# Performance work log

Measured on AMD Instinct MI355X. Metric: run time of the kernel, lower is better.

Reference implementation:

```python
import jax, jax.numpy as jnp
import numpy as np

B, T, D = 8, 2048, 1024
EPS = 1e-5

def _layernorm(x, g, b):
    mu = jnp.mean(x, axis=-1, keepdims=True)
    var = jnp.mean(jnp.square(x - mu), axis=-1, keepdims=True)
    return (x - mu) * jax.lax.rsqrt(var + EPS) * g + b

def setup_inputs() -> dict:
    key = jax.random.key(0)
    ks = jax.random.split(key, 8)
    scale = 1.0 / np.sqrt(D)
    text_inputs = jax.random.normal(ks[0], (B, T, D), dtype=jnp.float32)
    sit_mask = jax.random.randint(ks[1], (B, T), 0, 2).astype(jnp.float32)
    Wq = jax.random.normal(ks[2], (D, D), dtype=jnp.float32) * scale
    Wk = jax.random.normal(ks[3], (D, D), dtype=jnp.float32) * scale
    Wv = jax.random.normal(ks[4], (D, D), dtype=jnp.float32) * scale
    Wf1 = jax.random.normal(ks[5], (D, D), dtype=jnp.float32) * scale
    bf1 = jnp.zeros((D,), dtype=jnp.float32)
    Wf2 = jax.random.normal(ks[6], (D, D), dtype=jnp.float32) * scale
    bf2 = jnp.zeros((D,), dtype=jnp.float32)
    ln1_g = jnp.ones((D,), dtype=jnp.float32)
    ln1_b = jnp.zeros((D,), dtype=jnp.float32)
    ln2_g = jnp.ones((D,), dtype=jnp.float32)
    ln2_b = jnp.zeros((D,), dtype=jnp.float32)
    return dict(text_inputs=text_inputs, sit_mask=sit_mask, Wq=Wq, Wk=Wk, Wv=Wv,
                ln1_g=ln1_g, ln1_b=ln1_b, Wf1=Wf1, bf1=bf1, Wf2=Wf2, bf2=bf2,
                ln2_g=ln2_g, ln2_b=ln2_b)

def reference(text_inputs, sit_mask, Wq, Wk, Wv, ln1_g, ln1_b, Wf1, bf1, Wf2, bf2, ln2_g, ln2_b):
    x = text_inputs  # [B,T,D]
    d = x.shape[-1]
    # torch Linear: y = x @ W.T
    q = jnp.einsum('btd,ed->bte', x, Wq)
    k = jnp.einsum('btd,ed->bte', x, Wk)
    v = jnp.einsum('btd,ed->bte', x, Wv)
    # scaled scores with causal (strictly-upper = -inf) mask
    scores = jnp.einsum('btd,bsd->bts', q, k) / jnp.sqrt(jnp.asarray(d, x.dtype))
    causal = jnp.tril(jnp.ones((x.shape[1], x.shape[1]), dtype=bool))  # keep diag + past
    scores = jnp.where(causal[None], scores, -jnp.inf)
    attn = jax.nn.softmax(scores, axis=-1)
    # per-batch SIT padding mask applied AFTER softmax (rows may not sum to 1)
    pad_keep = (sit_mask[:, :, None] * sit_mask[:, None, :]) != 0  # [B,T,T]
    attn = jnp.where(pad_keep, attn, 0.0)
    att_out = jnp.einsum('bts,bsd->btd', attn, v)
    # residual + LN, FFN (Linear-ReLU-Linear), residual + LN
    h = _layernorm(att_out + x, ln1_g, ln1_b)
    ff = jnp.einsum('btd,ed->bte', jax.nn.relu(jnp.einsum('btd,ed->bte', h, Wf1) + bf1), Wf2) + bf2
    out = _layernorm(ff + h, ln2_g, ln2_b)
    return out
```

## Files before the change

### kernel.cpp

```cpp
#include <hip/hip_runtime.h>

typedef unsigned short ushort_t;
typedef __attribute__((ext_vector_type(8))) __bf16 bf16x8;
typedef __attribute__((ext_vector_type(4))) float f32x4;
typedef __attribute__((ext_vector_type(4))) int i32x4;
typedef __attribute__((ext_vector_type(4))) unsigned short u16x4;
typedef __attribute__((ext_vector_type(8))) unsigned short u16x8;

__device__ __forceinline__ float bf2f(ushort_t u) {
  union { unsigned u32; float f; } c; c.u32 = ((unsigned)u) << 16; return c.f;
}
__device__ __forceinline__ ushort_t f2bf(float f) {
  union { float f; unsigned u32; } c; c.f = f;
  unsigned u = c.u32;
  u += 0x7fffu + ((u >> 16) & 1u);
  return (ushort_t)(u >> 16);
}

__device__ __forceinline__ void gload_lds16(const void* g, void* l) {
  __builtin_amdgcn_global_load_lds(
      (const __attribute__((address_space(1))) void*)g,
      (__attribute__((address_space(3))) void*)l,
      16, 0, 0);
}

__device__ __forceinline__ void stage_half(const char* gbase, long row0, int ldbytes,
                                           int kbyte, char* lds_half, int tid)
{
  const int rl = tid >> 3;
  const int cs = ((tid & 7) ^ (rl & 7)) << 4;
  const char* g0 = gbase + (row0 + rl) * (long)ldbytes + kbyte + cs;
  char* l0 = lds_half + ((tid >> 6) << 10);
  gload_lds16(g0, l0);
  gload_lds16(g0 + (long)ldbytes * 64, l0 + 8192);
}

#define BAR() __builtin_amdgcn_s_barrier()
#define VMW4() asm volatile("s_waitcnt vmcnt(4)" ::: "memory")
#define VMW6() asm volatile("s_waitcnt vmcnt(6)" ::: "memory")
#define PR1() __builtin_amdgcn_s_setprio(1)
#define PR0() __builtin_amdgcn_s_setprio(0)

#define READ_A(dst, Abase, mb) \
  _Pragma("unroll") for (int m_ = 0; m_ < 4; ++m_) { \
    const char* p_ = (Abase) + ((wr << 7) + (mb) + m_ * 16 + fr) * 128; \
    dst[m_][0] = *(const bf16x8*)(p_ + ch0); \
    dst[m_][1] = *(const bf16x8*)(p_ + ch1); }

#define READ_B4(dst, Bbase, jb) \
  _Pragma("unroll") for (int n_ = 0; n_ < 2; ++n_) { \
    const char* p_ = (Bbase) + ((wc << 6) + (jb) + n_ * 16 + fr) * 128; \
    dst[n_][0] = *(const bf16x8*)(p_ + ch0); \
    dst[n_][1] = *(const bf16x8*)(p_ + ch1); }

#define MFMA_Q(ib, jb, aarr, barr) \
  _Pragma("unroll") for (int m_ = 0; m_ < 4; ++m_) \
  _Pragma("unroll") for (int n_ = 0; n_ < 2; ++n_) \
  _Pragma("unroll") for (int s_ = 0; s_ < 2; ++s_) \
    acc[(ib) + m_][(jb) + n_] = __builtin_amdgcn_mfma_f32_16x16x32_bf16( \
        aarr[m_][s_], barr[n_][s_], acc[(ib) + m_][(jb) + n_], 0, 0, 0);

#define STAGE_A(t, h, db) stage_half(gA, m0 + (h) * 128, ldab, (t) << 7, \
    (char*)lds + (db) * 32768 + (h) * 16384, tid)
#define STAGE_B(t, h, db) stage_half(gB, n0 + (h) * 128, ldbb, (t) << 7, \
    (char*)lds + 65536 + (db) * 32768 + (h) * 16384, tid)

template<int EPI, int MAPQ, bool ROUTE>
__global__ __launch_bounds__(512, 1) void gemm256(
    const ushort_t* __restrict__ A, int lda,
    const ushort_t* __restrict__ B, int ldb,
    ushort_t* __restrict__ C0, ushort_t* __restrict__ C1, ushort_t* __restrict__ C2,
    int ldc, const float* __restrict__ bias, float scale, int K)
{
  __shared__ __attribute__((aligned(16))) ushort_t lds[65536];

  int bx, by;
  if (MAPQ == 1) {
    const int flat = blockIdx.y * 4 + blockIdx.x;
    by = ((flat >> 5) << 3) | (flat & 7);
    bx = (flat >> 3) & 3;
  } else if (MAPQ == 2) {
    const int l = blockIdx.x;
    const int c = l & 7, u = l >> 3;
    const int q12 = u / 12;
    by = (q12 << 3) | c;
    bx = u - q12 * 12;
  } else { bx = blockIdx.x; by = blockIdx.y; }

  const int NT = K >> 6;
  const int NIT = NT >> 1, NTm1 = NT - 1;

  const int tid = threadIdx.x;
  const int lane = tid & 63, fr = lane & 15, g = lane >> 4, lm = lane & 7;
  const int wv = tid >> 6, wr = wv >> 2, wc = wv & 3;
  const long m0 = (long)by << 8, n0 = (long)bx << 8;

  const char* gA = (const char*)A;
  const char* gB = (const char*)B;
  const int ldab = lda << 1, ldbb = ldb << 1;

  const int ch0 = (g ^ lm) << 4;
  const int ch1 = ((4 | g) ^ lm) << 4;

  const char* A0 = (const char*)lds;
  const char* A1 = (const char*)lds + 32768;
  const char* B0 = (const char*)lds + 65536;
  const char* B1 = (const char*)lds + 98304;

  f32x4 acc[8][4] = {};
  bf16x8 aF[4][2], aG[4][2], bX[2][2];

  STAGE_A(0, 0, 0); STAGE_A(0, 1, 0); STAGE_B(0, 0, 0); STAGE_B(0, 1, 0);
  STAGE_A(1, 0, 1); STAGE_A(1, 1, 1);
  VMW4(); BAR();

  for (int i = 0; i < NIT; ++i) {
    const int t1 = 2 * i + 1;
    const int t2 = (2 * i + 2 < NTm1) ? 2 * i + 2 : NTm1;
    const int t3 = (2 * i + 3 < NTm1) ? 2 * i + 3 : NTm1;

    READ_A(aF, A0, 0); READ_B4(bX, B0, 0);
    STAGE_B(t1, 0, 1);
    BAR(); PR1(); MFMA_Q(0, 0, aF, bX); PR0(); BAR();

    READ_A(aG, A0, 64);
    STAGE_B(t1, 1, 1);
    BAR(); PR1(); MFMA_Q(4, 0, aG, bX); PR0(); BAR();

    READ_B4(bX, B0, 32);
    STAGE_A(t2, 0, 0);
    BAR(); PR1(); MFMA_Q(4, 2, aG, bX); PR0(); BAR();

    STAGE_A(t2, 1, 0);
    BAR(); PR1(); MFMA_Q(0, 2, aF, bX); PR0(); VMW4(); BAR();

    READ_A(aF, A1, 0); READ_B4(bX, B1, 0);
    STAGE_B(t2, 0, 0);
    BAR(); PR1(); MFMA_Q(0, 0, aF, bX); PR0(); BAR();

    READ_A(aG, A1, 64);
    STAGE_B(t2, 1, 0);
    BAR(); PR1(); MFMA_Q(4, 0, aG, bX); PR0(); BAR();

    READ_B4(bX, B1, 32);
    STAGE_A(t3, 0, 1);
    BAR(); PR1(); MFMA_Q(4, 2, aG, bX); PR0(); BAR();

    STAGE_A(t3, 1, 1);
    BAR(); PR1(); MFMA_Q(0, 2, aF, bX); PR0(); VMW4(); BAR();
  }

  ushort_t* Cd = C0;
  long nc0 = (long)bx << 8;
  if constexpr (ROUTE) {
    const int which = bx >> 2;
    Cd = (which == 0) ? C0 : (which == 1) ? C1 : C2;
    nc0 = (long)(bx & 3) << 8;
  }

  const int cm = g << 2, cn = fr;
#pragma unroll
  for (int i2 = 0; i2 < 8; ++i2)
#pragma unroll
    for (int j2 = 0; j2 < 4; ++j2) {
      const long gm = m0 + (wr << 7) + i2 * 16 + cm;
      const long gn = nc0 + (wc << 6) + j2 * 16 + cn;
      float bv = 0.f;
      if constexpr (EPI >= 1) bv = bias[gn];
#pragma unroll
      for (int r = 0; r < 4; ++r) {
        float v = acc[i2][j2][r] * scale + bv;
        if constexpr (EPI == 2) v = fmaxf(v, 0.f);
        Cd[(gm + r) * ldc + gn] = f2bf(v);
      }
    }
}

#define RDA4(dst, base, ch) \
  _Pragma("unroll") for (int m_ = 0; m_ < 4; ++m_) \
    dst[m_] = *(const bf16x8*)((base) + ((wr4 << 6) + m_ * 16 + fr) * 128 + (ch));

#define RDB4(dst, base, ch) \
  _Pragma("unroll") for (int n_ = 0; n_ < 4; ++n_) \
    dst[n_] = *(const bf16x8*)((base) + ((wc2 << 6) + n_ * 16 + fr) * 128 + (ch));

#define MM16() \
  _Pragma("unroll") for (int m_ = 0; m_ < 4; ++m_) \
  _Pragma("unroll") for (int n_ = 0; n_ < 4; ++n_) \
    acc[m_][n_] = __builtin_amdgcn_mfma_f32_16x16x32_bf16( \
        af[m_], bfv[n_], acc[m_][n_], 0, 0, 0);

#define SA2_(t, dst) do { \
    stage_half(gA, m0, ldab, (t) << 7, (dst), tid); \
    stage_half(gA, m0 + 128, ldab, (t) << 7, (dst) + 16384, tid); } while (0)
#define SB2_(t, dst) stage_half(gB, n0, ldbb, (t) << 7, (dst), tid)

template<int EPI, int MAP, bool CKLIM>
__global__ __launch_bounds__(512, 1) void gemmA(
    const ushort_t* __restrict__ A, int lda, long bsA,
    const ushort_t* __restrict__ B, int ldb, long bsB,
    ushort_t* __restrict__ C, int ldc, long bsC,
    const float* __restrict__ bias, float scale, int K)
{
  __shared__ __attribute__((aligned(16))) ushort_t lds[73728];

  int bx, by, bz;
  if (MAP == 1) {
    const int bid = blockIdx.x;
    bz = bid & 7; const int r = bid >> 3;
    by = 0; while ((by + 1) * (by + 2) <= r) ++by;
    bx = r - by * (by + 1);
  } else if (MAP == 2) {
    const int bid = blockIdx.x;
    bz = bid & 7; const int u = bid >> 3;
    by = 7 - (u >> 3); bx = u & 7;
  } else { bx = blockIdx.x; by = blockIdx.y; bz = blockIdx.z; }

  const int NT = CKLIM ? ((by + 1) << 2) : (K >> 6);

  const int tid = threadIdx.x;
  const int lane = tid & 63, fr = lane & 15, g = lane >> 4, lm = lane & 7;
  const int wv = tid >> 6;
  const int wr4 = wv >> 1, wc2 = wv & 1;
  const long m0 = (long)by << 8, n0 = (long)bx << 7;

  const char* gA = (const char*)(A + bz * bsA);
  const char* gB = (const char*)(B + bz * bsB);
  const int ldab = lda << 1, ldbb = ldb << 1;

  const int ch0 = (g ^ lm) << 4;
  const int ch1 = ((4 | g) ^ lm) << 4;

  char* a0 = (char*)lds;
  char* b0 = a0 + 32768;
  char* a1 = a0 + 49152;
  char* b1 = a1 + 32768;
  char* a2 = a0 + 98304;
  char* b2 = a2 + 32768;

  f32x4 acc[4][4] = {};
  bf16x8 af[4], bfv[4];

  SA2_(0, a0); SB2_(0, b0);
  SA2_(1, a1); SB2_(1, b1);
  VMW6(); BAR();

  for (int u = 0; u < NT; ++u) {
    const int t2 = (u + 2 < NT) ? u + 2 : NT - 1;
    RDA4(af, a0, ch0); RDB4(bfv, b0, ch0);
    SA2_(t2, a2); SB2_(t2, b2);
    BAR(); PR1(); MM16(); PR0(); BAR();
    RDA4(af, a0, ch1); RDB4(bfv, b0, ch1);
    VMW6(); BAR(); PR1(); MM16(); PR0(); BAR();
    char* ta = a0; a0 = a1; a1 = a2; a2 = ta;
    char* tb = b0; b0 = b1; b1 = b2; b2 = tb;
  }

  ushort_t* Cb = C + bz * bsC;
  const int cm = g << 2, cn = fr;
#pragma unroll
  for (int i2 = 0; i2 < 4; ++i2)
#pragma unroll
    for (int j2 = 0; j2 < 4; ++j2) {
      const long gm = m0 + (wr4 << 6) + i2 * 16 + cm;
      const long gn = n0 + (wc2 << 6) + j2 * 16 + cn;
      float bv = 0.f;
      if constexpr (EPI >= 1) bv = bias[gn];
#pragma unroll
      for (int r = 0; r < 4; ++r) {
        float v = acc[i2][j2][r] * scale + bv;
        if constexpr (EPI == 2) v = fmaxf(v, 0.f);
        Cb[(gm + r) * ldc + gn] = f2bf(v);
      }
    }
}

__global__ __launch_bounds__(256) void transpose_bf16(
    const ushort_t* __restrict__ V, int ldv, long bsV,
    ushort_t* __restrict__ Vt, int ldt, long bsT)
{
  __shared__ __attribute__((aligned(16))) ushort_t tile[64][72];
  const int bz = blockIdx.z;
  const ushort_t* Vb = V + bz * bsV;
  ushort_t* Tb = Vt + bz * bsT;
  const long s0 = (long)blockIdx.y << 6;
  const long d0 = (long)blockIdx.x << 6;
  const int tid = threadIdx.x;
  const int r = tid >> 3, c = tid & 7;
#pragma unroll
  for (int h = 0; h < 2; ++h) {
    const int rr = r + h * 32;
    i32x4 v = *(const i32x4*)(Vb + (s0 + rr) * ldv + d0 + c * 8);
    *(i32x4*)&tile[rr][c * 8] = v;
  }
  __syncthreads();
#pragma unroll
  for (int h = 0; h < 2; ++h) {
    const int dr = r + h * 32;
    union { ushort_t u[8]; i32x4 v; } t;
#pragma unroll
    for (int j = 0; j < 8; ++j) t.u[j] = tile[c * 8 + j][dr];
    *(i32x4*)(Tb + (d0 + dr) * ldt + s0 + c * 8) = t.v;
  }
}

__global__ __launch_bounds__(256) void softmax_sit(ushort_t* __restrict__ S,
                                                   const float* __restrict__ sit)
{
  __shared__ float red[4];
  const long row = blockIdx.x;
  const int b = (int)(row >> 11);
  const int t = (int)(row & 2047);
  const int n = t + 1;
  const int rup = ((t >> 8) + 1) << 8;
  ushort_t* Srow = S + (row << 11);
  const int tid = threadIdx.x;
  const int i0 = tid << 3;
  const bool act = i0 < rup;

  u16x8 raw = {};
  if (act) raw = *(const u16x8*)(Srow + i0);
  float v[8];
#pragma unroll
  for (int j = 0; j < 8; ++j) v[j] = bf2f(raw[j]);

  float mloc = -3.0e38f;
#pragma unroll
  for (int j = 0; j < 8; ++j) if (i0 + j < n) mloc = fmaxf(mloc, v[j]);
#pragma unroll
  for (int o = 32; o > 0; o >>= 1) mloc = fmaxf(mloc, __shfl_down(mloc, o, 64));
  if ((tid & 63) == 0) red[tid >> 6] = mloc;
  __syncthreads();
  const float m = fmaxf(fmaxf(red[0], red[1]), fmaxf(red[2], red[3]));
  __syncthreads();

  float e[8];
  float sloc = 0.f;
#pragma unroll
  for (int j = 0; j < 8; ++j) {
    e[j] = (i0 + j < n) ? __expf(v[j] - m) : 0.f;
    sloc += e[j];
  }
#pragma unroll
  for (int o = 32; o > 0; o >>= 1) sloc += __shfl_down(sloc, o, 64);
  if ((tid & 63) == 0) red[tid >> 6] = sloc;
  __syncthreads();
  const float l = red[0] + red[1] + red[2] + red[3];

  float inv = 1.f / l;
  if (sit[row] == 0.f) inv = 0.f;
  if (act) {
    const float* sitb = sit + ((long)b << 11) + i0;
    u16x8 out;
#pragma unroll
    for (int j = 0; j < 8; ++j) {
      const float p = (i0 + j < n && sitb[j] != 0.f) ? e[j] * inv : 0.f;
      out[j] = f2bf(p);
    }
    *(u16x8*)(Srow + i0) = out;
  }
}

template<bool RES_F32, bool OUT_F32>
__global__ __launch_bounds__(256) void resid_ln(
    const ushort_t* __restrict__ xin, const void* __restrict__ resv,
    const float* __restrict__ g, const float* __restrict__ be, void* __restrict__ outv)
{
  __shared__ float red[4];
  const long base = (long)blockIdx.x << 10;
  const int tid = threadIdx.x;
  const int i0 = tid << 2;

  const u16x4 xa = *(const u16x4*)(xin + base + i0);
  float v[4];
  if constexpr (RES_F32) {
    const float4 rv = *(const float4*)((const float*)resv + base + i0);
    v[0] = bf2f(xa.x) + rv.x; v[1] = bf2f(xa.y) + rv.y;
    v[2] = bf2f(xa.z) + rv.z; v[3] = bf2f(xa.w) + rv.w;
  } else {
    const u16x4 rb = *(const u16x4*)((const ushort_t*)resv + base + i0);
    v[0] = bf2f(xa.x) + bf2f(rb.x); v[1] = bf2f(xa.y) + bf2f(rb.y);
    v[2] = bf2f(xa.z) + bf2f(rb.z); v[3] = bf2f(xa.w) + bf2f(rb.w);
  }
  float s = v[0] + v[1] + v[2] + v[3];
#pragma unroll
  for (int o = 32; o > 0; o >>= 1) s += __shfl_down(s, o, 64);
  if ((tid & 63) == 0) red[tid >> 6] = s;
  __syncthreads();
  const float mu = (red[0] + red[1] + red[2] + red[3]) * (1.f / 1024.f);
  __syncthreads();
  float s2 = 0.f;
#pragma unroll
  for (int j = 0; j < 4; ++j) { const float d = v[j] - mu; s2 += d * d; }
#pragma unroll
  for (int o = 32; o > 0; o >>= 1) s2 += __shfl_down(s2, o, 64);
  if ((tid & 63) == 0) red[tid >> 6] = s2;
  __syncthreads();
  const float rstd = rsqrtf((red[0] + red[1] + red[2] + red[3]) * (1.f / 1024.f) + 1e-5f);

  const float4 gv = *(const float4*)(g + i0);
  const float4 bv = *(const float4*)(be + i0);
  const float o0 = (v[0] - mu) * rstd * gv.x + bv.x;
  const float o1 = (v[1] - mu) * rstd * gv.y + bv.y;
  const float o2 = (v[2] - mu) * rstd * gv.z + bv.z;
  const float o3 = (v[3] - mu) * rstd * gv.w + bv.w;
  if constexpr (OUT_F32) {
    float4 ov; ov.x = o0; ov.y = o1; ov.z = o2; ov.w = o3;
    *(float4*)((float*)outv + base + i0) = ov;
  } else {
    u16x4 ob = { f2bf(o0), f2bf(o1), f2bf(o2), f2bf(o3) };
    *(u16x4*)((ushort_t*)outv + base + i0) = ob;
  }
}

__global__ __launch_bounds__(256) void cast_f32_bf16(const float* __restrict__ src,
                                                     ushort_t* __restrict__ dst, int n4)
{
  const int i = blockIdx.x * 256 + threadIdx.x;
  if (i >= n4) return;
  const float4 v = *(const float4*)(src + ((long)i << 2));
  u16x4 o = { f2bf(v.x), f2bf(v.y), f2bf(v.z), f2bf(v.w) };
  *(u16x4*)(dst + ((long)i << 2)) = o;
}

__global__ __launch_bounds__(256) void cast_w5(
    const float* __restrict__ s0, const float* __restrict__ s1,
    const float* __restrict__ s2, const float* __restrict__ s3,
    const float* __restrict__ s4, ushort_t* __restrict__ dst)
{
  const int w = blockIdx.y;
  const float* src = (w == 0) ? s0 : (w == 1) ? s1 : (w == 2) ? s2 : (w == 3) ? s3 : s4;
  const long off = (long)w << 20;
  const int i = blockIdx.x * 256 + threadIdx.x;
  const float4 v = *(const float4*)(src + ((long)i << 2));
  u16x4 o = { f2bf(v.x), f2bf(v.y), f2bf(v.z), f2bf(v.w) };
  *(u16x4*)(dst + off + ((long)i << 2)) = o;
}

extern "C" void kernel_launch(void* const* d_in, const int* in_sizes, int n_in,
                              void* d_out, int out_size, void* d_ws, size_t ws_size,
                              hipStream_t stream) {
  const int T = 2048, D = 1024;
  const long TD = (long)T * D;
  const long ND = 8 * TD;
  const float* x    = (const float*)d_in[0];
  const float* sit  = (const float*)d_in[1];
  const float* Wq   = (const float*)d_in[2];
  const float* Wk   = (const float*)d_in[3];
  const float* Wv   = (const float*)d_in[4];
  const float* ln1g = (const float*)d_in[5];
  const float* ln1b = (const float*)d_in[6];
  const float* Wf1  = (const float*)d_in[7];
  const float* bf1  = (const float*)d_in[8];
  const float* Wf2  = (const float*)d_in[9];
  const float* bf2  = (const float*)d_in[10];
  const float* ln2g = (const float*)d_in[11];
  const float* ln2b = (const float*)d_in[12];

  ushort_t* W16 = (ushort_t*)d_ws;
  ushort_t* xb  = W16;
  ushort_t* vb  = W16 + ND;
  ushort_t* S   = W16;
  ushort_t* hb  = W16;
  ushort_t* ff1 = W16 + ND;
  ushort_t* vt  = W16 + 2 * ND;
  ushort_t* ff2 = vt;
  ushort_t* wq  = W16 + 3 * ND;
  ushort_t* wf1 = wq + 3L * D * D;
  ushort_t* wf2 = wf1 + (long)D * D;
  ushort_t* qb = (ushort_t*)d_out;
  ushort_t* kb = qb + ND;
  ushort_t* attb = (ushort_t*)d_out;

  cast_f32_bf16<<<16384, 256, 0, stream>>>(x, xb, (int)(ND / 4));
  cast_w5<<<dim3(1024, 5), 256, 0, stream>>>(Wq, Wk, Wv, Wf1, Wf2, wq);

  gemm256<0, 2, true><<<dim3(768), 512, 0, stream>>>(
      xb, 1024, wq, 1024, qb, kb, vb, 1024, nullptr, 1.f, 1024);

  transpose_bf16<<<dim3(16, 32, 8), 256, 0, stream>>>(vb, 1024, TD, vt, 2048, TD);

  gemmA<0, 1, false><<<dim3(576), 512, 0, stream>>>(
      qb, 1024, TD, kb, 1024, TD, S, 2048, (long)T * T, nullptr, 0.03125f, 1024);

  softmax_sit<<<16384, 256, 0, stream>>>(S, sit);

  gemmA<0, 2, true><<<dim3(512), 512, 0, stream>>>(
      S, 2048, (long)T * T, vt, 2048, TD, attb, 1024, TD, nullptr, 1.f, 2048);

  resid_ln<true, false><<<16384, 256, 0, stream>>>(attb, x, ln1g, ln1b, hb);

  gemm256<2, 1, false><<<dim3(4, 64), 512, 0, stream>>>(
      hb, 1024, wf1, 1024, ff1, ff1, ff1, 1024, bf1, 1.f, 1024);
  gemm256<1, 1, false><<<dim3(4, 64), 512, 0, stream>>>(
      ff1, 1024, wf2, 1024, ff2, ff2, ff2, 1024, bf2, 1.f, 1024);

  resid_ln<false, true><<<16384, 256, 0, stream>>>(ff2, hb, ln2g, ln2b, (float*)d_out);
}
```

Before: 395.6 us.

## Switch GEMM kernels to 32x32x16 MFMA with restructured software pipeline

Both GEMM kernels (the QKV/FFN gemm256 and the batched attention gemmA) move from 16x16x32 to 32x32x16 bf16 MFMA tiles. This lowers LDS fragment reads per FLOP and raises arithmetic intensity per instruction. The main loops are reordered so LDS fragment reads for the next quarter overlap the current MFMA group, and fragments are prefetched across barriers. Epilogues are rewritten for the 32x32 accumulator layout. The cost is higher register pressure and some risk in the new pipeline's waitcnt and barrier ordering, for example vmcnt(0) in gemm256.

```diff
diff --git a/kernel.cpp b/kernel.cpp
--- a/kernel.cpp
+++ b/kernel.cpp
@@ -2,6 +2,7 @@
 
 typedef unsigned short ushort_t;
 typedef __attribute__((ext_vector_type(8))) __bf16 bf16x8;
+typedef __attribute__((ext_vector_type(16))) float f32x16;
 typedef __attribute__((ext_vector_type(4))) float f32x4;
 typedef __attribute__((ext_vector_type(4))) int i32x4;
 typedef __attribute__((ext_vector_type(4))) unsigned short u16x4;
@@ -36,34 +37,28 @@
 }
 
 #define BAR() __builtin_amdgcn_s_barrier()
+#define VMW0() asm volatile("s_waitcnt vmcnt(0)" ::: "memory")
 #define VMW4() asm volatile("s_waitcnt vmcnt(4)" ::: "memory")
 #define VMW6() asm volatile("s_waitcnt vmcnt(6)" ::: "memory")
 #define PR1() __builtin_amdgcn_s_setprio(1)
 #define PR0() __builtin_amdgcn_s_setprio(0)
 
-#define READ_A(dst, Abase, mb) \
-  _Pragma("unroll") for (int m_ = 0; m_ < 4; ++m_) { \
-    const char* p_ = (Abase) + ((wr << 7) + (mb) + m_ * 16 + fr) * 128; \
-    dst[m_][0] = *(const bf16x8*)(p_ + ch0); \
-    dst[m_][1] = *(const bf16x8*)(p_ + ch1); }
-
-#define READ_B4(dst, Bbase, jb) \
-  _Pragma("unroll") for (int n_ = 0; n_ < 2; ++n_) { \
-    const char* p_ = (Bbase) + ((wc << 6) + (jb) + n_ * 16 + fr) * 128; \
-    dst[n_][0] = *(const bf16x8*)(p_ + ch0); \
-    dst[n_][1] = *(const bf16x8*)(p_ + ch1); }
-
-#define MFMA_Q(ib, jb, aarr, barr) \
-  _Pragma("unroll") for (int m_ = 0; m_ < 4; ++m_) \
-  _Pragma("unroll") for (int n_ = 0; n_ < 2; ++n_) \
-  _Pragma("unroll") for (int s_ = 0; s_ < 2; ++s_) \
-    acc[(ib) + m_][(jb) + n_] = __builtin_amdgcn_mfma_f32_16x16x32_bf16( \
-        aarr[m_][s_], barr[n_][s_], acc[(ib) + m_][(jb) + n_], 0, 0, 0);
-
-#define STAGE_A(t, h, db) stage_half(gA, m0 + (h) * 128, ldab, (t) << 7, \
-    (char*)lds + (db) * 32768 + (h) * 16384, tid)
-#define STAGE_B(t, h, db) stage_half(gB, n0 + (h) * 128, ldbb, (t) << 7, \
-    (char*)lds + 65536 + (db) * 32768 + (h) * 16384, tid)
+#define G_RA(dst, base, rb) \
+  _Pragma("unroll") for (int f_ = 0; f_ < 2; ++f_) \
+  _Pragma("unroll") for (int s_ = 0; s_ < 4; ++s_) \
+    dst[f_][s_] = *(const bf16x8*)((base) + ((rb) + f_ * 32 + l31) * 128 + ch[s_]);
+#define G_RB(dst, base, cb) \
+  _Pragma("unroll") for (int s_ = 0; s_ < 4; ++s_) \
+    dst[s_] = *(const bf16x8*)((base) + ((cb) + l31) * 128 + ch[s_]);
+#define G_MM(r0, nf, Aa, Bb) \
+  _Pragma("unroll") for (int s_ = 0; s_ < 4; ++s_) \
+  _Pragma("unroll") for (int f_ = 0; f_ < 2; ++f_) \
+    acc[(r0) + f_][nf] = __builtin_amdgcn_mfma_f32_32x32x16_bf16( \
+        Aa[f_][s_], Bb[s_], acc[(r0) + f_][nf], 0, 0, 0);
+#define SAE_(t, hh) stage_half(gA, m0 + (hh) * 128, ldab, (t) << 7, AE + (hh) * 16384, tid)
+#define SAO_(t, hh) stage_half(gA, m0 + (hh) * 128, ldab, (t) << 7, AO + (hh) * 16384, tid)
+#define SBE_(t, hh) stage_half(gB, n0 + (hh) * 128, ldbb, (t) << 7, BE + (hh) * 16384, tid)
+#define SBO_(t, hh) stage_half(gB, n0 + (hh) * 128, ldbb, (t) << 7, BO + (hh) * 16384, tid)
 
 template<int EPI, int MAPQ, bool ROUTE>
 __global__ __launch_bounds__(512, 1) void gemm256(
@@ -87,67 +82,68 @@
     bx = u - q12 * 12;
   } else { bx = blockIdx.x; by = blockIdx.y; }
 
-  const int NT = K >> 6;
-  const int NIT = NT >> 1, NTm1 = NT - 1;
-
-  const int tid = threadIdx.x;
-  const int lane = tid & 63, fr = lane & 15, g = lane >> 4, lm = lane & 7;
+  const int NT = K >> 6, NIT = NT >> 1, NTm1 = NT - 1;
+
+  const int tid = threadIdx.x, lane = tid & 63;
+  const int l31 = lane & 31, lm = lane & 7, h = lane >> 5;
   const int wv = tid >> 6, wr = wv >> 2, wc = wv & 3;
+  const int wrb = wr << 7, wcb = wc << 6;
   const long m0 = (long)by << 8, n0 = (long)bx << 8;
 
   const char* gA = (const char*)A;
   const char* gB = (const char*)B;
   const int ldab = lda << 1, ldbb = ldb << 1;
 
-  const int ch0 = (g ^ lm) << 4;
-  const int ch1 = ((4 | g) ^ lm) << 4;
-
-  const char* A0 = (const char*)lds;
-  const char* A1 = (const char*)lds + 32768;
-  const char* B0 = (const char*)lds + 65536;
-  const char* B1 = (const char*)lds + 98304;
-
-  f32x4 acc[8][4] = {};
-  bf16x8 aF[4][2], aG[4][2], bX[2][2];
-
-  STAGE_A(0, 0, 0); STAGE_A(0, 1, 0); STAGE_B(0, 0, 0); STAGE_B(0, 1, 0);
-  STAGE_A(1, 0, 1); STAGE_A(1, 1, 1);
+  int ch[4];
+#pragma unroll
+  for (int s = 0; s < 4; ++s) ch[s] = ((((s << 1) | h) ^ lm) << 4);
+
+  char* AE = (char*)lds;
+  char* AO = AE + 32768;
+  char* BE = AE + 65536;
+  char* BO = AE + 98304;
+
+  f32x16 acc[4][2] = {};
+  bf16x8 aF[2][4], aG[2][4], bL[4], bL2[4], bH[4];
+
+  SAE_(0, 0); SAE_(0, 1); SBE_(0, 0); SBE_(0, 1);
+  SAO_(1, 0); SAO_(1, 1);
   VMW4(); BAR();
+  G_RA(aF, AE, wrb); G_RB(bL, BE, wcb);
 
   for (int i = 0; i < NIT; ++i) {
-    const int t1 = 2 * i + 1;
+    const int tO = (2 * i + 1 < NTm1) ? 2 * i + 1 : NTm1;
     const int t2 = (2 * i + 2 < NTm1) ? 2 * i + 2 : NTm1;
     const int t3 = (2 * i + 3 < NTm1) ? 2 * i + 3 : NTm1;
 
-    READ_A(aF, A0, 0); READ_B4(bX, B0, 0);
-    STAGE_B(t1, 0, 1);
-    BAR(); PR1(); MFMA_Q(0, 0, aF, bX); PR0(); BAR();
-
-    READ_A(aG, A0, 64);
-    STAGE_B(t1, 1, 1);
-    BAR(); PR1(); MFMA_Q(4, 0, aG, bX); PR0(); BAR();
-
-    READ_B4(bX, B0, 32);
-    STAGE_A(t2, 0, 0);
-    BAR(); PR1(); MFMA_Q(4, 2, aG, bX); PR0(); BAR();
-
-    STAGE_A(t2, 1, 0);
-    BAR(); PR1(); MFMA_Q(0, 2, aF, bX); PR0(); VMW4(); BAR();
-
-    READ_A(aF, A1, 0); READ_B4(bX, B1, 0);
-    STAGE_B(t2, 0, 0);
-    BAR(); PR1(); MFMA_Q(0, 0, aF, bX); PR0(); BAR();
-
-    READ_A(aG, A1, 64);
-    STAGE_B(t2, 1, 0);
-    BAR(); PR1(); MFMA_Q(4, 0, aG, bX); PR0(); BAR();
-
-    READ_B4(bX, B1, 32);
-    STAGE_A(t3, 0, 1);
-    BAR(); PR1(); MFMA_Q(4, 2, aG, bX); PR0(); BAR();
-
-    STAGE_A(t3, 1, 1);
-    BAR(); PR1(); MFMA_Q(0, 2, aF, bX); PR0(); VMW4(); BAR();
+    PR1(); G_MM(0, 0, aF, bL); PR0();
+    G_RB(bH, BE, wcb + 32);
+    SBO_(tO, 0);
+    BAR();
+    PR1(); G_MM(0, 1, aF, bH); PR0();
+    G_RA(aG, AE, wrb + 64);
+    SBO_(tO, 1);
+    BAR();
+    PR1(); G_MM(2, 1, aG, bH); PR0();
+    BAR();
+    PR1(); G_MM(2, 0, aG, bL); PR0();
+    VMW0(); BAR();
+    G_RA(aF, AO, wrb); G_RB(bL2, BO, wcb);
+    SAE_(t2, 0); SAE_(t2, 1);
+    PR1(); G_MM(0, 0, aF, bL2); PR0();
+    G_RB(bH, BO, wcb + 32);
+    SBE_(t2, 0);
+    BAR();
+    PR1(); G_MM(0, 1, aF, bH); PR0();
+    G_RA(aG, AO, wrb + 64);
+    SBE_(t2, 1);
+    BAR();
+    PR1(); G_MM(2, 1, aG, bH); PR0();
+    BAR();
+    PR1(); G_MM(2, 0, aG, bL2); PR0();
+    VMW0(); BAR();
+    G_RA(aF, AE, wrb); G_RB(bL, BE, wcb);
+    SAO_(t3, 0); SAO_(t3, 1);
   }
 
   ushort_t* Cd = C0;
@@ -158,42 +154,34 @@
     nc0 = (long)(bx & 3) << 8;
   }
 
-  const int cm = g << 2, cn = fr;
-#pragma unroll
-  for (int i2 = 0; i2 < 8; ++i2)
-#pragma unroll
-    for (int j2 = 0; j2 < 4; ++j2) {
-      const long gm = m0 + (wr << 7) + i2 * 16 + cm;
-      const long gn = nc0 + (wc << 6) + j2 * 16 + cn;
+  const int rb4 = h << 2;
+#pragma unroll
+  for (int mf = 0; mf < 4; ++mf)
+#pragma unroll
+    for (int nf = 0; nf < 2; ++nf) {
+      const long gmb = m0 + wrb + mf * 32;
+      const long gn = nc0 + wcb + nf * 32 + l31;
       float bv = 0.f;
       if constexpr (EPI >= 1) bv = bias[gn];
 #pragma unroll
-      for (int r = 0; r < 4; ++r) {
-        float v = acc[i2][j2][r] * scale + bv;
+      for (int r = 0; r < 16; ++r) {
+        const int row = (r & 3) + 8 * (r >> 2) + rb4;
+        float v = acc[mf][nf][r] * scale + bv;
         if constexpr (EPI == 2) v = fmaxf(v, 0.f);
-        Cd[(gm + r) * ldc + gn] = f2bf(v);
+        Cd[(gmb + row) * ldc + gn] = f2bf(v);
       }
     }
 }
 
-#define RDA4(dst, base, ch) \
-  _Pragma("unroll") for (int m_ = 0; m_ < 4; ++m_) \
-    dst[m_] = *(const bf16x8*)((base) + ((wr4 << 6) + m_ * 16 + fr) * 128 + (ch));
-
-#define RDB4(dst, base, ch) \
-  _Pragma("unroll") for (int n_ = 0; n_ < 4; ++n_) \
-    dst[n_] = *(const bf16x8*)((base) + ((wc2 << 6) + n_ * 16 + fr) * 128 + (ch));
-
-#define MM16() \
-  _Pragma("unroll") for (int m_ = 0; m_ < 4; ++m_) \
-  _Pragma("unroll") for (int n_ = 0; n_ < 4; ++n_) \
-    acc[m_][n_] = __builtin_amdgcn_mfma_f32_16x16x32_bf16( \
-        af[m_], bfv[n_], acc[m_][n_], 0, 0, 0);
-
-#define SA2_(t, dst) do { \
-    stage_half(gA, m0, ldab, (t) << 7, (dst), tid); \
-    stage_half(gA, m0 + 128, ldab, (t) << 7, (dst) + 16384, tid); } while (0)
-#define SB2_(t, dst) stage_half(gB, n0, ldbb, (t) << 7, (dst), tid)
+#define A_RA(dst, base, rb) \
+  _Pragma("unroll") for (int s_ = 0; s_ < 4; ++s_) \
+    dst[s_] = *(const bf16x8*)((base) + ((rb) + l31) * 128 + ch[s_]);
+#define A_MM(mh, nh, Aa, Bb) \
+  _Pragma("unroll") for (int s_ = 0; s_ < 4; ++s_) \
+    acc[mh][nh] = __builtin_amdgcn_mfma_f32_32x32x16_bf16( \
+        Aa[s_], Bb[s_], acc[mh][nh], 0, 0, 0);
+#define SAA_(t, hh, dst) stage_half(gA, m0 + (hh) * 128, ldab, (t) << 7, (dst) + (hh) * 16384, tid)
+#define SBA_(t, dst) stage_half(gB, n0, ldbb, (t) << 7, (dst), tid)
 
 template<int EPI, int MAP, bool CKLIM>
 __global__ __launch_bounds__(512, 1) void gemmA(
@@ -217,60 +205,86 @@
   } else { bx = blockIdx.x; by = blockIdx.y; bz = blockIdx.z; }
 
   const int NT = CKLIM ? ((by + 1) << 2) : (K >> 6);
-
-  const int tid = threadIdx.x;
-  const int lane = tid & 63, fr = lane & 15, g = lane >> 4, lm = lane & 7;
-  const int wv = tid >> 6;
-  const int wr4 = wv >> 1, wc2 = wv & 1;
+  const int NIT = NT >> 1, NTm1 = NT - 1;
+
+  const int tid = threadIdx.x, lane = tid & 63;
+  const int l31 = lane & 31, lm = lane & 7, h = lane >> 5;
+  const int wv = tid >> 6, wr4 = wv >> 1, wc2 = wv & 1;
+  const int wrb = wr4 << 6, wcb = wc2 << 6;
   const long m0 = (long)by << 8, n0 = (long)bx << 7;
 
   const char* gA = (const char*)(A + bz * bsA);
   const char* gB = (const char*)(B + bz * bsB);
   const int ldab = lda << 1, ldbb = ldb << 1;
 
-  const int ch0 = (g ^ lm) << 4;
-  const int ch1 = ((4 | g) ^ lm) << 4;
-
-  char* a0 = (char*)lds;
-  char* b0 = a0 + 32768;
-  char* a1 = a0 + 49152;
-  char* b1 = a1 + 32768;
-  char* a2 = a0 + 98304;
-  char* b2 = a2 + 32768;
-
-  f32x4 acc[4][4] = {};
-  bf16x8 af[4], bfv[4];
-
-  SA2_(0, a0); SB2_(0, b0);
-  SA2_(1, a1); SB2_(1, b1);
+  int ch[4];
+#pragma unroll
+  for (int s = 0; s < 4; ++s) ch[s] = ((((s << 1) | h) ^ lm) << 4);
+
+  char* pA0 = (char*)lds;          char* pB0 = pA0 + 32768;
+  char* pA1 = (char*)lds + 49152;  char* pB1 = pA1 + 32768;
+  char* pA2 = (char*)lds + 98304;  char* pB2 = pA2 + 32768;
+
+  f32x16 acc[2][2] = {};
+  bf16x8 aF[4], aG[4], bL[4], bL2[4], bH[4];
+
+  SAA_(0, 0, pA0); SAA_(0, 1, pA0); SBA_(0, pB0);
+  SAA_(1, 0, pA1); SAA_(1, 1, pA1); SBA_(1, pB1);
   VMW6(); BAR();
-
-  for (int u = 0; u < NT; ++u) {
-    const int t2 = (u + 2 < NT) ? u + 2 : NT - 1;
-    RDA4(af, a0, ch0); RDB4(bfv, b0, ch0);
-    SA2_(t2, a2); SB2_(t2, b2);
-    BAR(); PR1(); MM16(); PR0(); BAR();
-    RDA4(af, a0, ch1); RDB4(bfv, b0, ch1);
-    VMW6(); BAR(); PR1(); MM16(); PR0(); BAR();
-    char* ta = a0; a0 = a1; a1 = a2; a2 = ta;
-    char* tb = b0; b0 = b1; b1 = b2; b2 = tb;
+  A_RA(aF, pA0, wrb); A_RA(bL, pB0, wcb);
+
+  for (int i = 0; i < NIT; ++i) {
+    const int t2 = (2 * i + 2 < NTm1) ? 2 * i + 2 : NTm1;
+    const int t3 = (2 * i + 3 < NTm1) ? 2 * i + 3 : NTm1;
+
+    PR1(); A_MM(0, 0, aF, bL); PR0();
+    A_RA(bH, pB0, wcb + 32);
+    SAA_(t2, 0, pA2);
+    BAR();
+    PR1(); A_MM(0, 1, aF, bH); PR0();
+    A_RA(aG, pA0, wrb + 32);
+    SAA_(t2, 1, pA2);
+    BAR();
+    PR1(); A_MM(1, 1, aG, bH); PR0();
+    SBA_(t2, pB2);
+    BAR();
+    PR1(); A_MM(1, 0, aG, bL); PR0();
+    VMW6(); BAR();
+    A_RA(aF, pA1, wrb); A_RA(bL2, pB1, wcb);
+    PR1(); A_MM(0, 0, aF, bL2); PR0();
+    A_RA(bH, pB1, wcb + 32);
+    SAA_(t3, 0, pA0);
+    BAR();
+    PR1(); A_MM(0, 1, aF, bH); PR0();
+    A_RA(aG, pA1, wrb + 32);
+    SAA_(t3, 1, pA0);
+    BAR();
+    PR1(); A_MM(1, 1, aG, bH); PR0();
+    SBA_(t3, pB0);
+    BAR();
+    PR1(); A_MM(1, 0, aG, bL2); PR0();
+    VMW6(); BAR();
+    A_RA(aF, pA2, wrb); A_RA(bL, pB2, wcb);
+    char* tA = pA0; pA0 = pA2; pA2 = pA1; pA1 = tA;
+    char* tB = pB0; pB0 = pB2; pB2 = pB1; pB1 = tB;
   }
 
   ushort_t* Cb = C + bz * bsC;
-  const int cm = g << 2, cn = fr;
-#pragma unroll
-  for (int i2 = 0; i2 < 4; ++i2)
-#pragma unroll
-    for (int j2 = 0; j2 < 4; ++j2) {
-      const long gm = m0 + (wr4 << 6) + i2 * 16 + cm;
-      const long gn = n0 + (wc2 << 6) + j2 * 16 + cn;
+  const int rb4 = h << 2;
+#pragma unroll
+  for (int mf = 0; mf < 2; ++mf)
+#pragma unroll
+    for (int nf = 0; nf < 2; ++nf) {
+      const long gmb = m0 + wrb + mf * 32;
+      const long gn = n0 + wcb + nf * 32 + l31;
       float bv = 0.f;
       if constexpr (EPI >= 1) bv = bias[gn];
 #pragma unroll
-      for (int r = 0; r < 4; ++r) {
-        float v = acc[i2][j2][r] * scale + bv;
+      for (int r = 0; r < 16; ++r) {
+        const int row = (r & 3) + 8 * (r >> 2) + rb4;
+        float v = acc[mf][nf][r] * scale + bv;
         if constexpr (EPI == 2) v = fmaxf(v, 0.f);
-        Cb[(gm + r) * ldc + gn] = f2bf(v);
+        Cb[(gmb + row) * ldc + gn] = f2bf(v);
       }
     }
 }
@@ -288,15 +302,15 @@
   const int tid = threadIdx.x;
   const int r = tid >> 3, c = tid & 7;
 #pragma unroll
-  for (int h = 0; h < 2; ++h) {
-    const int rr = r + h * 32;
+  for (int hh = 0; hh < 2; ++hh) {
+    const int rr = r + hh * 32;
     i32x4 v = *(const i32x4*)(Vb + (s0 + rr) * ldv + d0 + c * 8);
     *(i32x4*)&tile[rr][c * 8] = v;
   }
   __syncthreads();
 #pragma unroll
-  for (int h = 0; h < 2; ++h) {
-    const int dr = r + h * 32;
+  for (int hh = 0; hh < 2; ++hh) {
+    const int dr = r + hh * 32;
     union { ushort_t u[8]; i32x4 v; } t;
 #pragma unroll
     for (int j = 0; j < 8; ++j) t.u[j] = tile[c * 8 + j][dr];
```

New measurement: 397.9 us. Within noise of the previous version (+0.6%).

## Restructure GEMM main loops into ping-pong pipelines with early LDS fragment reads

Applied to the files above, without the earlier changes.

Both GEMM kernels (gemm256 and gemmA) get a new main loop. Each now processes two K-tiles per iteration and loads the next tile's fragments from LDS before the barrier. B fragments are split into low and high halves, so MFMA quadrants start on data already in registers while the other half loads. gemm256 moves to a full A+B even/odd double buffer, staged after compute with vmcnt(8). gemmA keeps a 3-buffer rotation but unrolls by two, splits the full-K reads per fragment, and interleaves global->LDS staging between MFMA groups. The aim is to hide LDS read latency and cut barrier stalls, at the cost of more live registers, and it assumes an even tile count NT.

```diff
diff --git a/kernel.cpp b/kernel.cpp
--- a/kernel.cpp
+++ b/kernel.cpp
@@ -36,34 +36,32 @@
 }
 
 #define BAR() __builtin_amdgcn_s_barrier()
-#define VMW4() asm volatile("s_waitcnt vmcnt(4)" ::: "memory")
 #define VMW6() asm volatile("s_waitcnt vmcnt(6)" ::: "memory")
+#define VMW8() asm volatile("s_waitcnt vmcnt(8)" ::: "memory")
 #define PR1() __builtin_amdgcn_s_setprio(1)
 #define PR0() __builtin_amdgcn_s_setprio(0)
 
-#define READ_A(dst, Abase, mb) \
+#define RD_A4(dst, base, rb) \
   _Pragma("unroll") for (int m_ = 0; m_ < 4; ++m_) { \
-    const char* p_ = (Abase) + ((wr << 7) + (mb) + m_ * 16 + fr) * 128; \
+    const char* p_ = (base) + ((rb) + m_ * 16 + fr) * 128; \
     dst[m_][0] = *(const bf16x8*)(p_ + ch0); \
     dst[m_][1] = *(const bf16x8*)(p_ + ch1); }
-
-#define READ_B4(dst, Bbase, jb) \
+#define RD_B2(dst, base, cb) \
   _Pragma("unroll") for (int n_ = 0; n_ < 2; ++n_) { \
-    const char* p_ = (Bbase) + ((wc << 6) + (jb) + n_ * 16 + fr) * 128; \
+    const char* p_ = (base) + ((cb) + n_ * 16 + fr) * 128; \
     dst[n_][0] = *(const bf16x8*)(p_ + ch0); \
     dst[n_][1] = *(const bf16x8*)(p_ + ch1); }
 
-#define MFMA_Q(ib, jb, aarr, barr) \
+#define G_MM(ib, jb, Aa, Bb) \
   _Pragma("unroll") for (int m_ = 0; m_ < 4; ++m_) \
   _Pragma("unroll") for (int n_ = 0; n_ < 2; ++n_) \
   _Pragma("unroll") for (int s_ = 0; s_ < 2; ++s_) \
     acc[(ib) + m_][(jb) + n_] = __builtin_amdgcn_mfma_f32_16x16x32_bf16( \
-        aarr[m_][s_], barr[n_][s_], acc[(ib) + m_][(jb) + n_], 0, 0, 0);
-
-#define STAGE_A(t, h, db) stage_half(gA, m0 + (h) * 128, ldab, (t) << 7, \
-    (char*)lds + (db) * 32768 + (h) * 16384, tid)
-#define STAGE_B(t, h, db) stage_half(gB, n0 + (h) * 128, ldbb, (t) << 7, \
-    (char*)lds + 65536 + (db) * 32768 + (h) * 16384, tid)
+        Aa[m_][s_], Bb[n_][s_], acc[(ib) + m_][(jb) + n_], 0, 0, 0);
+#define SAE_(t, hh) stage_half(gA, m0 + (hh) * 128, ldab, (t) << 7, AE + (hh) * 16384, tid)
+#define SAO_(t, hh) stage_half(gA, m0 + (hh) * 128, ldab, (t) << 7, AO + (hh) * 16384, tid)
+#define SBE_(t, hh) stage_half(gB, n0 + (hh) * 128, ldbb, (t) << 7, BE + (hh) * 16384, tid)
+#define SBO_(t, hh) stage_half(gB, n0 + (hh) * 128, ldbb, (t) << 7, BO + (hh) * 16384, tid)
 
 template<int EPI, int MAPQ, bool ROUTE>
 __global__ __launch_bounds__(512, 1) void gemm256(
@@ -87,12 +85,12 @@
     bx = u - q12 * 12;
   } else { bx = blockIdx.x; by = blockIdx.y; }
 
-  const int NT = K >> 6;
-  const int NIT = NT >> 1, NTm1 = NT - 1;
-
-  const int tid = threadIdx.x;
-  const int lane = tid & 63, fr = lane & 15, g = lane >> 4, lm = lane & 7;
+  const int NT = K >> 6, NIT = NT >> 1, NTm1 = NT - 1;
+
+  const int tid = threadIdx.x, lane = tid & 63;
+  const int fr = lane & 15, g = lane >> 4, lm = lane & 7;
   const int wv = tid >> 6, wr = wv >> 2, wc = wv & 3;
+  const int wrb = wr << 7, wcb = wc << 6;
   const long m0 = (long)by << 8, n0 = (long)bx << 8;
 
   const char* gA = (const char*)A;
@@ -102,52 +100,47 @@
   const int ch0 = (g ^ lm) << 4;
   const int ch1 = ((4 | g) ^ lm) << 4;
 
-  const char* A0 = (const char*)lds;
-  const char* A1 = (const char*)lds + 32768;
-  const char* B0 = (const char*)lds + 65536;
-  const char* B1 = (const char*)lds + 98304;
+  char* AE = (char*)lds;
+  char* AO = AE + 32768;
+  char* BE = AE + 65536;
+  char* BO = AE + 98304;
 
   f32x4 acc[8][4] = {};
-  bf16x8 aF[4][2], aG[4][2], bX[2][2];
-
-  STAGE_A(0, 0, 0); STAGE_A(0, 1, 0); STAGE_B(0, 0, 0); STAGE_B(0, 1, 0);
-  STAGE_A(1, 0, 1); STAGE_A(1, 1, 1);
-  VMW4(); BAR();
+  bf16x8 aF[4][2], aG[4][2], bL[2][2], bL2[2][2], bH[2][2];
+
+  SAE_(0, 0); SAE_(0, 1); SBE_(0, 0); SBE_(0, 1);
+  SAO_(1, 0); SAO_(1, 1); SBO_(1, 0); SBO_(1, 1);
+  VMW8(); BAR();
+  RD_A4(aF, AE, wrb); RD_B2(bL, BE, wcb);
 
   for (int i = 0; i < NIT; ++i) {
-    const int t1 = 2 * i + 1;
     const int t2 = (2 * i + 2 < NTm1) ? 2 * i + 2 : NTm1;
     const int t3 = (2 * i + 3 < NTm1) ? 2 * i + 3 : NTm1;
 
-    READ_A(aF, A0, 0); READ_B4(bX, B0, 0);
-    STAGE_B(t1, 0, 1);
-    BAR(); PR1(); MFMA_Q(0, 0, aF, bX); PR0(); BAR();
-
-    READ_A(aG, A0, 64);
-    STAGE_B(t1, 1, 1);
-    BAR(); PR1(); MFMA_Q(4, 0, aG, bX); PR0(); BAR();
-
-    READ_B4(bX, B0, 32);
-    STAGE_A(t2, 0, 0);
-    BAR(); PR1(); MFMA_Q(4, 2, aG, bX); PR0(); BAR();
-
-    STAGE_A(t2, 1, 0);
-    BAR(); PR1(); MFMA_Q(0, 2, aF, bX); PR0(); VMW4(); BAR();
-
-    READ_A(aF, A1, 0); READ_B4(bX, B1, 0);
-    STAGE_B(t2, 0, 0);
-    BAR(); PR1(); MFMA_Q(0, 0, aF, bX); PR0(); BAR();
-
-    READ_A(aG, A1, 64);
-    STAGE_B(t2, 1, 0);
-    BAR(); PR1(); MFMA_Q(4, 0, aG, bX); PR0(); BAR();
-
-    READ_B4(bX, B1, 32);
-    STAGE_A(t3, 0, 1);
-    BAR(); PR1(); MFMA_Q(4, 2, aG, bX); PR0(); BAR();
-
-    STAGE_A(t3, 1, 1);
-    BAR(); PR1(); MFMA_Q(0, 2, aF, bX); PR0(); VMW4(); BAR();
+    PR1(); G_MM(0, 0, aF, bL); PR0();
+    RD_B2(bH, BE, wcb + 32);
+    BAR();
+    PR1(); G_MM(0, 2, aF, bH); PR0();
+    RD_A4(aG, AE, wrb + 64);
+    BAR();
+    PR1(); G_MM(4, 2, aG, bH); PR0();
+    BAR();
+    PR1(); G_MM(4, 0, aG, bL); PR0();
+    SAE_(t2, 0); SAE_(t2, 1); SBE_(t2, 0); SBE_(t2, 1);
+    VMW8(); BAR();
+    RD_A4(aF, AO, wrb); RD_B2(bL2, BO, wcb);
+    PR1(); G_MM(0, 0, aF, bL2); PR0();
+    RD_B2(bH, BO, wcb + 32);
+    BAR();
+    PR1(); G_MM(0, 2, aF, bH); PR0();
+    RD_A4(aG, AO, wrb + 64);
+    BAR();
+    PR1(); G_MM(4, 2, aG, bH); PR0();
+    BAR();
+    PR1(); G_MM(4, 0, aG, bL2); PR0();
+    SAO_(t3, 0); SAO_(t3, 1); SBO_(t3, 0); SBO_(t3, 1);
+    VMW8(); BAR();
+    RD_A4(aF, AE, wrb); RD_B2(bL, BE, wcb);
   }
 
   ushort_t* Cd = C0;
@@ -163,8 +156,8 @@
   for (int i2 = 0; i2 < 8; ++i2)
 #pragma unroll
     for (int j2 = 0; j2 < 4; ++j2) {
-      const long gm = m0 + (wr << 7) + i2 * 16 + cm;
-      const long gn = nc0 + (wc << 6) + j2 * 16 + cn;
+      const long gm = m0 + wrb + i2 * 16 + cm;
+      const long gn = nc0 + wcb + j2 * 16 + cn;
       float bv = 0.f;
       if constexpr (EPI >= 1) bv = bias[gn];
 #pragma unroll
@@ -176,24 +169,14 @@
     }
 }
 
-#define RDA4(dst, base, ch) \
+#define A_MM(jb, Aa, Bb) \
   _Pragma("unroll") for (int m_ = 0; m_ < 4; ++m_) \
-    dst[m_] = *(const bf16x8*)((base) + ((wr4 << 6) + m_ * 16 + fr) * 128 + (ch));
-
-#define RDB4(dst, base, ch) \
-  _Pragma("unroll") for (int n_ = 0; n_ < 4; ++n_) \
-    dst[n_] = *(const bf16x8*)((base) + ((wc2 << 6) + n_ * 16 + fr) * 128 + (ch));
-
-#define MM16() \
-  _Pragma("unroll") for (int m_ = 0; m_ < 4; ++m_) \
-  _Pragma("unroll") for (int n_ = 0; n_ < 4; ++n_) \
-    acc[m_][n_] = __builtin_amdgcn_mfma_f32_16x16x32_bf16( \
-        af[m_], bfv[n_], acc[m_][n_], 0, 0, 0);
-
-#define SA2_(t, dst) do { \
-    stage_half(gA, m0, ldab, (t) << 7, (dst), tid); \
-    stage_half(gA, m0 + 128, ldab, (t) << 7, (dst) + 16384, tid); } while (0)
-#define SB2_(t, dst) stage_half(gB, n0, ldbb, (t) << 7, (dst), tid)
+  _Pragma("unroll") for (int n_ = 0; n_ < 2; ++n_) \
+  _Pragma("unroll") for (int s_ = 0; s_ < 2; ++s_) \
+    acc[m_][(jb) + n_] = __builtin_amdgcn_mfma_f32_16x16x32_bf16( \
+        Aa[m_][s_], Bb[n_][s_], acc[m_][(jb) + n_], 0, 0, 0);
+#define SAA_(t, hh, dst) stage_half(gA, m0 + (hh) * 128, ldab, (t) << 7, (dst) + (hh) * 16384, tid)
+#define SBA_(t, dst) stage_half(gB, n0, ldbb, (t) << 7, (dst), tid)
 
 template<int EPI, int MAP, bool CKLIM>
 __global__ __launch_bounds__(512, 1) void gemmA(
@@ -217,11 +200,12 @@
   } else { bx = blockIdx.x; by = blockIdx.y; bz = blockIdx.z; }
 
   const int NT = CKLIM ? ((by + 1) << 2) : (K >> 6);
-
-  const int tid = threadIdx.x;
-  const int lane = tid & 63, fr = lane & 15, g = lane >> 4, lm = lane & 7;
-  const int wv = tid >> 6;
-  const int wr4 = wv >> 1, wc2 = wv & 1;
+  const int NIT = NT >> 1, NTm1 = NT - 1;
+
+  const int tid = threadIdx.x, lane = tid & 63;
+  const int fr = lane & 15, g = lane >> 4, lm = lane & 7;
+  const int wv = tid >> 6, wr4 = wv >> 1, wc2 = wv & 1;
+  const int wrb = wr4 << 6, wcb = wc2 << 6;
   const long m0 = (long)by << 8, n0 = (long)bx << 7;
 
   const char* gA = (const char*)(A + bz * bsA);
@@ -231,29 +215,40 @@
   const int ch0 = (g ^ lm) << 4;
   const int ch1 = ((4 | g) ^ lm) << 4;
 
-  char* a0 = (char*)lds;
-  char* b0 = a0 + 32768;
-  char* a1 = a0 + 49152;
-  char* b1 = a1 + 32768;
-  char* a2 = a0 + 98304;
-  char* b2 = a2 + 32768;
+  char* pEA = (char*)lds;          char* pEB = pEA + 32768;
+  char* pOA = (char*)lds + 49152;  char* pOB = pOA + 32768;
+  char* pSA = (char*)lds + 98304;  char* pSB = pSA + 32768;
 
   f32x4 acc[4][4] = {};
-  bf16x8 af[4], bfv[4];
-
-  SA2_(0, a0); SB2_(0, b0);
-  SA2_(1, a1); SB2_(1, b1);
+  bf16x8 aE[4][2], aO[4][2], bLE[2][2], bLO[2][2], bH[2][2];
+
+  SAA_(0, 0, pEA); SAA_(0, 1, pEA); SBA_(0, pEB);
+  SAA_(1, 0, pOA); SAA_(1, 1, pOA); SBA_(1, pOB);
   VMW6(); BAR();
-
-  for (int u = 0; u < NT; ++u) {
-    const int t2 = (u + 2 < NT) ? u + 2 : NT - 1;
-    RDA4(af, a0, ch0); RDB4(bfv, b0, ch0);
-    SA2_(t2, a2); SB2_(t2, b2);
-    BAR(); PR1(); MM16(); PR0(); BAR();
-    RDA4(af, a0, ch1); RDB4(bfv, b0, ch1);
-    VMW6(); BAR(); PR1(); MM16(); PR0(); BAR();
-    char* ta = a0; a0 = a1; a1 = a2; a2 = ta;
-    char* tb = b0; b0 = b1; b1 = b2; b2 = tb;
+  RD_A4(aE, pEA, wrb); RD_B2(bLE, pEB, wcb);
+
+  for (int i = 0; i < NIT; ++i) {
+    const int t2 = (2 * i + 2 < NTm1) ? 2 * i + 2 : NTm1;
+    const int t3 = (2 * i + 3 < NTm1) ? 2 * i + 3 : NTm1;
+
+    PR1(); A_MM(0, aE, bLE); PR0();
+    RD_B2(bH, pEB, wcb + 32);
+    SAA_(t2, 0, pSA); SAA_(t2, 1, pSA);
+    BAR();
+    PR1(); A_MM(2, aE, bH); PR0();
+    SBA_(t2, pSB);
+    VMW6(); BAR();
+    RD_A4(aO, pOA, wrb); RD_B2(bLO, pOB, wcb);
+    PR1(); A_MM(0, aO, bLO); PR0();
+    RD_B2(bH, pOB, wcb + 32);
+    SAA_(t3, 0, pEA); SAA_(t3, 1, pEA);
+    BAR();
+    PR1(); A_MM(2, aO, bH); PR0();
+    SBA_(t3, pEB);
+    VMW6(); BAR();
+    RD_A4(aE, pSA, wrb); RD_B2(bLE, pSB, wcb);
+    char* tA = pEA; pEA = pSA; pSA = pOA; pOA = tA;
+    char* tB = pEB; pEB = pSB; pSB = pOB; pOB = tB;
   }
 
   ushort_t* Cb = C + bz * bsC;
@@ -262,8 +257,8 @@
   for (int i2 = 0; i2 < 4; ++i2)
 #pragma unroll
     for (int j2 = 0; j2 < 4; ++j2) {
-      const long gm = m0 + (wr4 << 6) + i2 * 16 + cm;
-      const long gn = n0 + (wc2 << 6) + j2 * 16 + cn;
+      const long gm = m0 + wrb + i2 * 16 + cm;
+      const long gn = n0 + wcb + j2 * 16 + cn;
       float bv = 0.f;
       if constexpr (EPI >= 1) bv = bias[gn];
 #pragma unroll
@@ -288,15 +283,15 @@
   const int tid = threadIdx.x;
   const int r = tid >> 3, c = tid & 7;
 #pragma unroll
-  for (int h = 0; h < 2; ++h) {
-    const int rr = r + h * 32;
+  for (int hh = 0; hh < 2; ++hh) {
+    const int rr = r + hh * 32;
     i32x4 v = *(const i32x4*)(Vb + (s0 + rr) * ldv + d0 + c * 8);
     *(i32x4*)&tile[rr][c * 8] = v;
   }
   __syncthreads();
 #pragma unroll
-  for (int h = 0; h < 2; ++h) {
-    const int dr = r + h * 32;
+  for (int hh = 0; hh < 2; ++hh) {
+    const int dr = r + hh * 32;
     union { ushort_t u[8]; i32x4 v; } t;
 #pragma unroll
     for (int j = 0; j < 8; ++j) t.u[j] = tile[c * 8 + j][dr];
```

Result: no change. 394.0 us (-0.4%).
